# Kernel tuning notes

Measured on AMD Instinct MI355X. Metric: run time of the kernel, lower is better.

## Reference

```python
import jax, jax.numpy as jnp
import numpy as np

NQ = 12          # n_qubits
DEPTH = 8        # vqc_depth
NCLASS = 10      # n_class
BATCH = 4096
DIM = 2 ** NQ    # statevector dimension


def _ry(theta):
    # RY(theta) = [[cos(t/2), -sin(t/2)], [sin(t/2), cos(t/2)]] (real)
    c = jnp.cos(theta / 2)
    s = jnp.sin(theta / 2)
    return jnp.stack([jnp.stack([c, -s], -1), jnp.stack([s, c], -1)], -2)


def _apply_1q(state, U, q):
    # state: [B, DIM] real; wire 0 = most-significant bit (PennyLane convention)
    B = state.shape[0]
    L = 2 ** q
    R = DIM // (2 * L)
    s = state.reshape(B, L, 2, R)
    if U.ndim == 2:   # shared gate
        s = jnp.einsum('ij,bljr->blir', U, s)
    else:             # per-sample gate [B,2,2]
        s = jnp.einsum('bij,bljr->blir', U, s)
    return s.reshape(B, DIM)


def _cnot_adj(state, i):
    # CNOT with control=i, target=i+1 (adjacent wires)
    B = state.shape[0]
    L = 2 ** i
    R = DIM // (4 * L)
    s = state.reshape(B, L, 2, 2, R)
    # control=0 block unchanged; control=1 block has target amplitudes swapped
    s = jnp.concatenate([s[:, :, :1], s[:, :, 1:, ::-1]], axis=2)
    return s.reshape(B, DIM)


def _vqc(X, weights):
    B = X.shape[0]
    # H on every wire applied to |0...0> gives the uniform positive state
    state = jnp.full((B, DIM), 2.0 ** (-NQ / 2), dtype=X.dtype)
    # data-encoding RY layer (per-sample angles)
    for q in range(NQ):
        state = _apply_1q(state, _ry(X[:, q]), q)
    # variational layers
    for k in range(DEPTH):
        for i in range(0, NQ - 1, 2):
            state = _cnot_adj(state, i)
        for i in range(1, NQ - 1, 2):
            state = _cnot_adj(state, i)
        for q in range(NQ):
            state = _apply_1q(state, _ry(weights[k, q]), q)
    # <Z_p> = P(bit p = 0) - P(bit p = 1); amplitudes are real
    probs = state * state  # [B, DIM]
    outs = []
    for p in range(NCLASS):
        L = 2 ** p
        R = DIM // (2 * L)
        pr = probs.reshape(B, L, 2, R)
        outs.append((pr[:, :, 0] - pr[:, :, 1]).sum(axis=(1, 2)))
    return jnp.stack(outs, axis=1)  # [B, NCLASS]


def setup_inputs() -> dict:
    key = jax.random.key(0)
    kx, kw = jax.random.split(key)
    X = jax.random.normal(kx, (BATCH, NQ), dtype=jnp.float32)
    weights = 0.01 * jax.random.normal(kw, (DEPTH, NQ), dtype=jnp.float32)
    return {"X": X, "weights": weights}


def reference(X, weights):
    return _vqc(X, weights)
```

## Files before the change

### kernel.cpp

```cpp
#include <hip/hip_runtime.h>
#include <hip/hip_fp16.h>

#define NQ 12
#define DEPTH 8
#define NCLASS 10
#define BATCH 4096
#define LSTRIDE 68
#define WPB 2


__device__ __forceinline__ uint32_t h2u(__half2 x) { return __builtin_bit_cast(uint32_t, x); }
__device__ __forceinline__ __half2 u2h(uint32_t x) { return __builtin_bit_cast(__half2, x); }

__device__ constexpr int hfun(int r) {
    const int rb5 = (r >> 5) & 1, rb4 = (r >> 4) & 1, rb3 = (r >> 3) & 1;
    const int rb2 = (r >> 2) & 1, rb1 = (r >> 1) & 1, rb0 = r & 1;
    const int c0 = rb5;
    const int c1 = rb4 ^ rb5;
    const int c2 = rb3 ^ rb4;
    const int c3 = rb2 ^ rb3 ^ rb4;
    const int c4 = rb1 ^ rb2;
    const int c5 = rb0 ^ rb1 ^ rb2;
    return (c0 << 5) | (c1 << 4) | (c2 << 3) | (c3 << 2) | (c4 << 1) | c5;
}

template <int M>
__device__ __forceinline__ void shear16(__half2 (&v)[64], __half2 T2, __half2 Tn2) {
#pragma unroll
    for (int r = 0; r < 64; ++r) {
        if (r & M) continue;
        const int r1 = r | M;
        const __half2 a = v[r], b = v[r1];
        v[r]  = __hfma2(Tn2, b, a);
        v[r1] = __hfma2(T2, a, b);
    }
}

__global__ __launch_bounds__(WPB * 64) void vqc_kernel(const float* __restrict__ X,
                                                       const float* __restrict__ W,
                                                       float* __restrict__ out) {
    __shared__ __align__(16) uint32_t lds[WPB * 64 * LSTRIDE];

    const int lane = threadIdx.x & 63;
    const int wid  = threadIdx.x >> 6;
    const int gw   = blockIdx.x * WPB + wid;
    const int s0   = 2 * gw, s1 = s0 + 1;
    const int l    = lane;

    uint32_t* Wb   = &lds[wid * 64 * LSTRIDE];
    uint32_t* wrow = &Wb[l * LSTRIDE];
    const int G = l ^ (l >> 1) ^ ((l >> 2) & 5);
    const uint32_t* colA = &Wb[G];
    const uint32_t* colB = &Wb[G ^ 0x30];
    const uint32_t* rT2  = &Wb[l];

    float cx0[NQ], sx0[NQ], cx1[NQ], sx1[NQ];
#pragma unroll
    for (int q = 0; q < NQ; ++q) {
        __sincosf(0.5f * X[s0 * NQ + q] + 0.78539816339744831f, &sx0[q], &cx0[q]);
        __sincosf(0.5f * X[s1 * NQ + q] + 0.78539816339744831f, &sx1[q], &cx1[q]);
    }
    float P0 = 1.0f, P1 = 1.0f;
#pragma unroll
    for (int q = 0; q < 6; ++q) {
        P0 *= ((l >> (5 - q)) & 1) ? sx0[q] : cx0[q];
        P1 *= ((l >> (5 - q)) & 1) ? sx1[q] : cx1[q];
    }

    __half2 v[64];
    v[0] = __floats2half2_rn(P0 * cx0[11], P1 * cx1[11]);
    v[1] = __floats2half2_rn(P0 * sx0[11], P1 * sx1[11]);
#pragma unroll
    for (int lvl = 1; lvl < 6; ++lvl) {
        const int q = 11 - lvl;
        const __half2 SX = __floats2half2_rn(sx0[q], sx1[q]);
        const __half2 CX = __floats2half2_rn(cx0[q], cx1[q]);
#pragma unroll
        for (int j = 0; j < (1 << 5); ++j) {
            if (j >= (1 << lvl)) continue;
            v[j + (1 << lvl)] = __hmul2(v[j], SX);
            v[j]              = __hmul2(v[j], CX);
        }
    }

    float Call = 1.0f;

#pragma unroll 1
    for (int k = 0; k < DEPTH; ++k) {
#pragma unroll
        for (int t = 0; t < 16; ++t) {
            uint4 w = make_uint4(h2u(v[4 * t]), h2u(v[4 * t + 1]),
                                 h2u(v[4 * t + 2]), h2u(v[4 * t + 3]));
            *(uint4*)&wrow[4 * t] = w;
        }
#pragma unroll
        for (int r = 0; r < 64; ++r)
            v[r] = u2h(((r & 1) ? colB : colA)[hfun(r) * LSTRIDE]);

#pragma unroll
        for (int p = 0; p < 6; ++p) {
            float cw, sw;
            __sincosf(0.5f * W[k * NQ + p], &sw, &cw);
            Call *= cw;
            const float t = sw / cw;
            const __half2 T2  = __floats2half2_rn(t, t);
            const __half2 Tn2 = __floats2half2_rn(-t, -t);
            switch (p) {
                case 0: shear16<32>(v, T2, Tn2); break;
                case 1: shear16<16>(v, T2, Tn2); break;
                case 2: shear16<8>(v, T2, Tn2); break;
                case 3: shear16<4>(v, T2, Tn2); break;
                case 4: shear16<2>(v, T2, Tn2); break;
                case 5: shear16<1>(v, T2, Tn2); break;
            }
        }

#pragma unroll
        for (int t = 0; t < 16; ++t) {
            uint4 w = make_uint4(h2u(v[4 * t]), h2u(v[4 * t + 1]),
                                 h2u(v[4 * t + 2]), h2u(v[4 * t + 3]));
            *(uint4*)&wrow[4 * t] = w;
        }
#pragma unroll
        for (int j = 0; j < 64; ++j)
            v[j] = u2h(rT2[j * LSTRIDE]);

#pragma unroll
        for (int p = 6; p < NQ; ++p) {
            float cw, sw;
            __sincosf(0.5f * W[k * NQ + p], &sw, &cw);
            Call *= cw;
            const float t = sw / cw;
            const __half2 T2  = __floats2half2_rn(t, t);
            const __half2 Tn2 = __floats2half2_rn(-t, -t);
            switch (p) {
                case 6:  shear16<32>(v, T2, Tn2); break;
                case 7:  shear16<16>(v, T2, Tn2); break;
                case 8:  shear16<8>(v, T2, Tn2); break;
                case 9:  shear16<4>(v, T2, Tn2); break;
                case 10: shear16<2>(v, T2, Tn2); break;
                case 11: shear16<1>(v, T2, Tn2); break;
            }
        }
    }

    const float C2 = (Call * Call);

    float c20[16], c21[16];
#pragma unroll
    for (int m = 0; m < 16; ++m) {
        float a0 = 0.0f, a1 = 0.0f;
#pragma unroll
        for (int i = 0; i < 4; ++i) {
            const float2 f = __half22float2(v[4 * m + i]);
            a0 += f.x * f.x;
            a1 += f.y * f.y;
        }
        c20[m] = a0;
        c21[m] = a1;
    }

    float S0 = 0.0f, S1 = 0.0f;
#pragma unroll
    for (int m = 0; m < 16; ++m) { S0 += c20[m]; S1 += c21[m]; }
    S0 *= C2; S1 *= C2;

    float T0[4], T1[4];
#pragma unroll
    for (int t = 0; t < 4; ++t) {
        float a0 = 0.0f, a1 = 0.0f;
#pragma unroll
        for (int m = 0; m < 16; ++m) {
            const float sgn = ((m >> t) & 1) ? -1.0f : 1.0f;
            a0 += sgn * c20[m];
            a1 += sgn * c21[m];
        }
        T0[t] = a0 * C2;
        T1[t] = a1 * C2;
    }

    float o0[NCLASS], o1[NCLASS];
#pragma unroll
    for (int p = 0; p < 6; ++p) {
        const float sgn = ((l >> (5 - p)) & 1) ? -1.0f : 1.0f;
        float r0 = sgn * S0, r1 = sgn * S1;
#pragma unroll
        for (int m = 0; m < 6; ++m) { r0 += __shfl_xor(r0, 1 << m, 64); r1 += __shfl_xor(r1, 1 << m, 64); }
        o0[p] = r0; o1[p] = r1;
    }
#pragma unroll
    for (int p = 6; p < 10; ++p) {
        float r0 = T0[9 - p], r1 = T1[9 - p];
#pragma unroll
        for (int m = 0; m < 6; ++m) { r0 += __shfl_xor(r0, 1 << m, 64); r1 += __shfl_xor(r1, 1 << m, 64); }
        o0[p] = r0; o1[p] = r1;
    }

    if (lane == 0) {
#pragma unroll
        for (int p = 0; p < NCLASS; ++p) {
            out[s0 * NCLASS + p] = o0[p];
            out[s1 * NCLASS + p] = o1[p];
        }
    }
}

extern "C" void kernel_launch(void* const* d_in, const int* in_sizes, int n_in,
                              void* d_out, int out_size, void* d_ws, size_t ws_size,
                              hipStream_t stream) {
    const float* X = (const float*)d_in[0];
    const float* W = (const float*)d_in[1];
    float* out     = (float*)d_out;
    (void)in_sizes; (void)n_in; (void)out_size; (void)d_ws; (void)ws_size;

    dim3 grid(BATCH / (2 * WPB));
    dim3 block(WPB * 64);
    hipLaunchKernelGGL(vqc_kernel, grid, block, 0, stream, X, W, out);
}
```

Before: 97.17 us.

## Map one sample per wavefront with half2 packing qubit 11 and permlane swaps

Each wavefront now simulates one sample instead of two. The lowest qubit is packed into the two halves of each half2, so each lane holds 32 registers instead of 64. The qubit-0 rotation moves to cross-half permlane32 swaps and the qubit-11 rotation to in-register half swaps, which shrinks the LDS transposes and the register footprint. It also sets launch bounds for four blocks per CU to raise occupancy. The grid doubles, and the extra lane-level shuffles and half swaps add instructions per sample in exchange.

```diff
diff --git a/kernel.cpp b/kernel.cpp
--- a/kernel.cpp
+++ b/kernel.cpp
@@ -5,215 +5,219 @@
 #define DEPTH 8
 #define NCLASS 10
 #define BATCH 4096
-#define LSTRIDE 68
+#define LSTR 36
 #define WPB 2
 
 
-__device__ __forceinline__ uint32_t h2u(__half2 x) { return __builtin_bit_cast(uint32_t, x); }
-__device__ __forceinline__ __half2 u2h(uint32_t x) { return __builtin_bit_cast(__half2, x); }
-
-__device__ constexpr int hfun(int r) {
-    const int rb5 = (r >> 5) & 1, rb4 = (r >> 4) & 1, rb3 = (r >> 3) & 1;
-    const int rb2 = (r >> 2) & 1, rb1 = (r >> 1) & 1, rb0 = r & 1;
-    const int c0 = rb5;
-    const int c1 = rb4 ^ rb5;
-    const int c2 = rb3 ^ rb4;
-    const int c3 = rb2 ^ rb3 ^ rb4;
-    const int c4 = rb1 ^ rb2;
-    const int c5 = rb0 ^ rb1 ^ rb2;
-    return (c0 << 5) | (c1 << 4) | (c2 << 3) | (c3 << 2) | (c4 << 1) | c5;
-}
-
-template <int M>
-__device__ __forceinline__ void shear16(__half2 (&v)[64], __half2 T2, __half2 Tn2) {
-#pragma unroll
-    for (int r = 0; r < 64; ++r) {
-        if (r & M) continue;
+typedef unsigned int u32;
+
+__device__ __forceinline__ u32 h2u(__half2 x){ return __builtin_bit_cast(u32, x); }
+__device__ __forceinline__ __half2 u2h(u32 x){ return __builtin_bit_cast(__half2, x); }
+
+__device__ constexpr int sigma_pa(int c){
+    const int c4=(c>>4)&1, c3=(c>>3)&1, c2=(c>>2)&1, c1=(c>>1)&1, c0=c&1;
+    return (c4<<4) | ((c3^c4)<<3) | ((c2^c3)<<2) | ((c1^c2^c3)<<1) | (c0^c1);
+}
+__device__ constexpr int swap_pa(int c){ return (c ^ (c>>1)) & 1; }
+
+__device__ constexpr int rowlow_pt(int r){
+    const int r4=(r>>4)&1, r3=(r>>3)&1, r2=(r>>2)&1, r1=(r>>1)&1, r0=r&1;
+    return ((r3^r4)<<3) | ((r2^r3^r4)<<2) | ((r1^r2)<<1) | (r0^r1^r2);
+}
+
+template<int M>
+__device__ __forceinline__ void shear(__half2 (&v)[32], __half2 T2, __half2 Tn2){
+#pragma unroll
+    for(int r=0;r<32;++r){
+        if(r & M) continue;
         const int r1 = r | M;
         const __half2 a = v[r], b = v[r1];
         v[r]  = __hfma2(Tn2, b, a);
-        v[r1] = __hfma2(T2, a, b);
-    }
-}
-
-__global__ __launch_bounds__(WPB * 64) void vqc_kernel(const float* __restrict__ X,
-                                                       const float* __restrict__ W,
-                                                       float* __restrict__ out) {
-    __shared__ __align__(16) uint32_t lds[WPB * 64 * LSTRIDE];
+        v[r1] = __hfma2(T2,  a, b);
+    }
+}
+
+__global__ __launch_bounds__(WPB*64, 4) void vqc_kernel(const float* __restrict__ X,
+                                                        const float* __restrict__ W,
+                                                        float* __restrict__ out){
+    __shared__ __align__(16) u32 lds[WPB*64*LSTR];
 
     const int lane = threadIdx.x & 63;
     const int wid  = threadIdx.x >> 6;
-    const int gw   = blockIdx.x * WPB + wid;
-    const int s0   = 2 * gw, s1 = s0 + 1;
-    const int l    = lane;
-
-    uint32_t* Wb   = &lds[wid * 64 * LSTRIDE];
-    uint32_t* wrow = &Wb[l * LSTRIDE];
-    const int G = l ^ (l >> 1) ^ ((l >> 2) & 5);
-    const uint32_t* colA = &Wb[G];
-    const uint32_t* colB = &Wb[G ^ 0x30];
-    const uint32_t* rT2  = &Wb[l];
-
-    float cx0[NQ], sx0[NQ], cx1[NQ], sx1[NQ];
-#pragma unroll
-    for (int q = 0; q < NQ; ++q) {
-        __sincosf(0.5f * X[s0 * NQ + q] + 0.78539816339744831f, &sx0[q], &cx0[q]);
-        __sincosf(0.5f * X[s1 * NQ + q] + 0.78539816339744831f, &sx1[q], &cx1[q]);
-    }
-    float P0 = 1.0f, P1 = 1.0f;
-#pragma unroll
-    for (int q = 0; q < 6; ++q) {
-        P0 *= ((l >> (5 - q)) & 1) ? sx0[q] : cx0[q];
-        P1 *= ((l >> (5 - q)) & 1) ? sx1[q] : cx1[q];
-    }
-
-    __half2 v[64];
-    v[0] = __floats2half2_rn(P0 * cx0[11], P1 * cx1[11]);
-    v[1] = __floats2half2_rn(P0 * sx0[11], P1 * sx1[11]);
-#pragma unroll
-    for (int lvl = 1; lvl < 6; ++lvl) {
-        const int q = 11 - lvl;
-        const __half2 SX = __floats2half2_rn(sx0[q], sx1[q]);
-        const __half2 CX = __floats2half2_rn(cx0[q], cx1[q]);
-#pragma unroll
-        for (int j = 0; j < (1 << 5); ++j) {
-            if (j >= (1 << lvl)) continue;
-            v[j + (1 << lvl)] = __hmul2(v[j], SX);
-            v[j]              = __hmul2(v[j], CX);
+    const int s    = blockIdx.x*WPB + wid;
+
+    u32* Wb   = &lds[wid*64*LSTR];
+    u32* wrow = &Wb[lane*LSTR];
+    const int l5  = lane >> 5;
+    const int lo5 = lane & 31;
+    const u32* p00 = &Wb[(l5?0x30:0x00)*LSTR +  lo5      ];
+    const u32* p01 = &Wb[(l5?0x30:0x00)*LSTR + (lo5^16)  ];
+    const u32* p10 = &Wb[(l5?0x20:0x10)*LSTR +  lo5      ];
+    const u32* p11 = &Wb[(l5?0x20:0x10)*LSTR + (lo5^16)  ];
+    const u32* rT2 = &Wb[(lane&32)*LSTR + lo5];
+
+    float cx[NQ], sx[NQ];
+#pragma unroll
+    for(int q=0;q<NQ;++q)
+        __sincosf(0.5f*X[s*NQ+q] + 0.78539816339744831f, &sx[q], &cx[q]);
+
+    float P = 1.0f;
+#pragma unroll
+    for(int q=0;q<6;++q) P *= ((lane>>(5-q))&1) ? sx[q] : cx[q];
+
+    __half2 v[32];
+    v[0] = __floats2half2_rn(P*cx[11], P*sx[11]);
+#pragma unroll
+    for(int lvl=0;lvl<5;++lvl){
+        const int q = 10 - lvl;
+        const __half2 SX = __float2half2_rn(sx[q]);
+        const __half2 CX = __float2half2_rn(cx[q]);
+#pragma unroll
+        for(int j=0;j<16;++j){
+            if(j >= (1<<lvl)) continue;
+            v[j+(1<<lvl)] = __hmul2(v[j], SX);
+            v[j]          = __hmul2(v[j], CX);
         }
     }
 
     float Call = 1.0f;
 
+#define PAV(c) (swap_pa(c) ? h2u(__lowhigh2highlow(v[sigma_pa(c)])) : h2u(v[sigma_pa(c)]))
+
 #pragma unroll 1
-    for (int k = 0; k < DEPTH; ++k) {
-#pragma unroll
-        for (int t = 0; t < 16; ++t) {
-            uint4 w = make_uint4(h2u(v[4 * t]), h2u(v[4 * t + 1]),
-                                 h2u(v[4 * t + 2]), h2u(v[4 * t + 3]));
-            *(uint4*)&wrow[4 * t] = w;
-        }
-#pragma unroll
-        for (int r = 0; r < 64; ++r)
-            v[r] = u2h(((r & 1) ? colB : colA)[hfun(r) * LSTRIDE]);
-
-#pragma unroll
-        for (int p = 0; p < 6; ++p) {
+    for(int k=0;k<DEPTH;++k){
+        const float* Wk = &W[k*NQ];
+
+#pragma unroll
+        for(int t=0;t<8;++t){
+            uint4 w = make_uint4(PAV(4*t+0), PAV(4*t+1), PAV(4*t+2), PAV(4*t+3));
+            *(uint4*)&wrow[4*t] = w;
+        }
+#pragma unroll
+        for(int r=0;r<32;++r){
+            const u32* pp = (r&16) ? ((r&1)?p11:p10) : ((r&1)?p01:p00);
+            v[r] = u2h(pp[rowlow_pt(r)*LSTR]);
+        }
+
+        {
             float cw, sw;
-            __sincosf(0.5f * W[k * NQ + p], &sw, &cw);
+#pragma unroll
+            for(int q=1;q<6;++q){
+                __sincosf(0.5f*Wk[q], &sw, &cw);
+                Call *= cw;
+                const float tq = sw/cw;
+                const __half2 T2  = __floats2half2_rn(tq, tq);
+                const __half2 Tn2 = __floats2half2_rn(-tq, -tq);
+                switch(q){
+                    case 1: shear<16>(v,T2,Tn2); break;
+                    case 2: shear<8>(v,T2,Tn2);  break;
+                    case 3: shear<4>(v,T2,Tn2);  break;
+                    case 4: shear<2>(v,T2,Tn2);  break;
+                    case 5: shear<1>(v,T2,Tn2);  break;
+                }
+            }
+        }
+
+        {
+            float cw, sw;
+            __sincosf(0.5f*Wk[0], &sw, &cw);
             Call *= cw;
-            const float t = sw / cw;
-            const __half2 T2  = __floats2half2_rn(t, t);
-            const __half2 Tn2 = __floats2half2_rn(-t, -t);
-            switch (p) {
-                case 0: shear16<32>(v, T2, Tn2); break;
-                case 1: shear16<16>(v, T2, Tn2); break;
-                case 2: shear16<8>(v, T2, Tn2); break;
-                case 3: shear16<4>(v, T2, Tn2); break;
-                case 4: shear16<2>(v, T2, Tn2); break;
-                case 5: shear16<1>(v, T2, Tn2); break;
+            const float tq = sw/cw;
+            const __half2 Tp = __floats2half2_rn(tq, tq);
+            const __half2 Tn = __floats2half2_rn(-tq, -tq);
+            const __half2 Tsgn = l5 ? Tp : Tn;
+#pragma unroll
+            for(int r=0;r<32;++r){
+                u32 a = h2u(v[r]), b = a;
+                asm("v_permlane32_swap_b32 %0, %1" : "+v"(a), "+v"(b));
+                const u32 x = l5 ? a : b;
+                v[r] = __hfma2(Tsgn, u2h(x), v[r]);
             }
         }
 
 #pragma unroll
-        for (int t = 0; t < 16; ++t) {
-            uint4 w = make_uint4(h2u(v[4 * t]), h2u(v[4 * t + 1]),
-                                 h2u(v[4 * t + 2]), h2u(v[4 * t + 3]));
-            *(uint4*)&wrow[4 * t] = w;
-        }
-#pragma unroll
-        for (int j = 0; j < 64; ++j)
-            v[j] = u2h(rT2[j * LSTRIDE]);
-
-#pragma unroll
-        for (int p = 6; p < NQ; ++p) {
+        for(int t=0;t<8;++t){
+            uint4 w = make_uint4(h2u(v[4*t]), h2u(v[4*t+1]), h2u(v[4*t+2]), h2u(v[4*t+3]));
+            *(uint4*)&wrow[4*t] = w;
+        }
+#pragma unroll
+        for(int r=0;r<32;++r) v[r] = u2h(rT2[r*LSTR]);
+
+        {
             float cw, sw;
-            __sincosf(0.5f * W[k * NQ + p], &sw, &cw);
+#pragma unroll
+            for(int q=6;q<11;++q){
+                __sincosf(0.5f*Wk[q], &sw, &cw);
+                Call *= cw;
+                const float tq = sw/cw;
+                const __half2 T2  = __floats2half2_rn(tq, tq);
+                const __half2 Tn2 = __floats2half2_rn(-tq, -tq);
+                switch(q){
+                    case 6:  shear<16>(v,T2,Tn2); break;
+                    case 7:  shear<8>(v,T2,Tn2);  break;
+                    case 8:  shear<4>(v,T2,Tn2);  break;
+                    case 9:  shear<2>(v,T2,Tn2);  break;
+                    case 10: shear<1>(v,T2,Tn2);  break;
+                }
+            }
+            __sincosf(0.5f*Wk[11], &sw, &cw);
             Call *= cw;
-            const float t = sw / cw;
-            const __half2 T2  = __floats2half2_rn(t, t);
-            const __half2 Tn2 = __floats2half2_rn(-t, -t);
-            switch (p) {
-                case 6:  shear16<32>(v, T2, Tn2); break;
-                case 7:  shear16<16>(v, T2, Tn2); break;
-                case 8:  shear16<8>(v, T2, Tn2); break;
-                case 9:  shear16<4>(v, T2, Tn2); break;
-                case 10: shear16<2>(v, T2, Tn2); break;
-                case 11: shear16<1>(v, T2, Tn2); break;
-            }
-        }
-    }
-
-    const float C2 = (Call * Call);
-
-    float c20[16], c21[16];
-#pragma unroll
-    for (int m = 0; m < 16; ++m) {
-        float a0 = 0.0f, a1 = 0.0f;
-#pragma unroll
-        for (int i = 0; i < 4; ++i) {
-            const float2 f = __half22float2(v[4 * m + i]);
-            a0 += f.x * f.x;
-            a1 += f.y * f.y;
-        }
-        c20[m] = a0;
-        c21[m] = a1;
-    }
-
-    float S0 = 0.0f, S1 = 0.0f;
-#pragma unroll
-    for (int m = 0; m < 16; ++m) { S0 += c20[m]; S1 += c21[m]; }
-    S0 *= C2; S1 *= C2;
-
-    float T0[4], T1[4];
-#pragma unroll
-    for (int t = 0; t < 4; ++t) {
-        float a0 = 0.0f, a1 = 0.0f;
-#pragma unroll
-        for (int m = 0; m < 16; ++m) {
-            const float sgn = ((m >> t) & 1) ? -1.0f : 1.0f;
-            a0 += sgn * c20[m];
-            a1 += sgn * c21[m];
-        }
-        T0[t] = a0 * C2;
-        T1[t] = a1 * C2;
-    }
-
-    float o0[NCLASS], o1[NCLASS];
-#pragma unroll
-    for (int p = 0; p < 6; ++p) {
-        const float sgn = ((l >> (5 - p)) & 1) ? -1.0f : 1.0f;
-        float r0 = sgn * S0, r1 = sgn * S1;
-#pragma unroll
-        for (int m = 0; m < 6; ++m) { r0 += __shfl_xor(r0, 1 << m, 64); r1 += __shfl_xor(r1, 1 << m, 64); }
-        o0[p] = r0; o1[p] = r1;
-    }
-#pragma unroll
-    for (int p = 6; p < 10; ++p) {
-        float r0 = T0[9 - p], r1 = T1[9 - p];
-#pragma unroll
-        for (int m = 0; m < 6; ++m) { r0 += __shfl_xor(r0, 1 << m, 64); r1 += __shfl_xor(r1, 1 << m, 64); }
-        o0[p] = r0; o1[p] = r1;
-    }
-
-    if (lane == 0) {
-#pragma unroll
-        for (int p = 0; p < NCLASS; ++p) {
-            out[s0 * NCLASS + p] = o0[p];
-            out[s1 * NCLASS + p] = o1[p];
-        }
+            const float tq = sw/cw;
+            const __half2 Tpm = __floats2half2_rn(-tq, tq);
+#pragma unroll
+            for(int r=0;r<32;++r)
+                v[r] = __hfma2(Tpm, __lowhigh2highlow(v[r]), v[r]);
+        }
+    }
+#undef PAV
+
+    const float C2 = Call*Call;
+    float Sall = 0.f, Tb[4] = {0.f,0.f,0.f,0.f};
+#pragma unroll
+    for(int r=0;r<32;++r){
+        const float2 f = __half22float2(v[r]);
+        const float c2 = f.x*f.x + f.y*f.y;
+        Sall += c2;
+        Tb[0] += ((r>>4)&1) ? -c2 : c2;
+        Tb[1] += ((r>>3)&1) ? -c2 : c2;
+        Tb[2] += ((r>>2)&1) ? -c2 : c2;
+        Tb[3] += ((r>>1)&1) ? -c2 : c2;
+    }
+    Sall *= C2;
+#pragma unroll
+    for(int j=0;j<4;++j) Tb[j] *= C2;
+
+    float o[NCLASS];
+#pragma unroll
+    for(int p=0;p<6;++p){
+        float rr = (((lane>>(5-p))&1) ? -Sall : Sall);
+#pragma unroll
+        for(int m=0;m<6;++m) rr += __shfl_xor(rr, 1<<m, 64);
+        o[p] = rr;
+    }
+#pragma unroll
+    for(int p=6;p<NCLASS;++p){
+        float rr = Tb[p-6];
+#pragma unroll
+        for(int m=0;m<6;++m) rr += __shfl_xor(rr, 1<<m, 64);
+        o[p] = rr;
+    }
+
+    if(lane == 0){
+#pragma unroll
+        for(int p=0;p<NCLASS;++p) out[s*NCLASS+p] = o[p];
     }
 }
 
 extern "C" void kernel_launch(void* const* d_in, const int* in_sizes, int n_in,
                               void* d_out, int out_size, void* d_ws, size_t ws_size,
-                              hipStream_t stream) {
+                              hipStream_t stream){
     const float* X = (const float*)d_in[0];
     const float* W = (const float*)d_in[1];
     float* out     = (float*)d_out;
     (void)in_sizes; (void)n_in; (void)out_size; (void)d_ws; (void)ws_size;
 
-    dim3 grid(BATCH / (2 * WPB));
+    dim3 grid(BATCH / WPB);
     dim3 block(WPB * 64);
     hipLaunchKernelGGL(vqc_kernel, grid, block, 0, stream, X, W, out);
 }
```

After: 107.1 us. 10.3% more time.
